# Optimization experiments

Measured on AMD Instinct MI355X. Metric: run time of the kernel, lower is better.

Reference implementation:

```python
import jax, jax.numpy as jnp
import numpy as np

THRESHOLD = 0.1  # init kwarg threshold
N_HITS_PER_EVENT = 200000
N_EVENTS = 64


def setup_inputs() -> dict:
    key = jax.random.key(0)
    n = N_HITS_PER_EVENT * N_EVENTS
    score = jax.random.uniform(key, (n, 1), dtype=jnp.float32)  # noise score in (0,1)
    row_splits = (jnp.arange(N_EVENTS + 1, dtype=jnp.int32) * N_HITS_PER_EVENT)
    return {"score": score, "row_splits": row_splits}


def reference(score, row_splits):
    """Faithful, fully vectorized version of select_threshold_with_backgather.

    Per segment: keep all vertices with score > threshold PLUS all vertices tied
    with the segment minimum score; non-kept vertices backgather to the FIRST
    kept minimum-score vertex of their segment (new/compacted indexing).
    Returns (sel [M,1], newrs [n_seg+1], backgather [N,1]) in the layer's
    call-output order (sel, newrs, allbackgather).
    """
    s = score[:, 0]
    n = s.shape[0]
    n_seg = row_splits.shape[0] - 1

    # segment id of every vertex from the row splits
    segids = jnp.searchsorted(row_splits, jnp.arange(n, dtype=row_splits.dtype), side='right') - 1
    segids = segids.astype(jnp.int32)

    # per-segment minimum score; ties with the min are all kept (== original isminscore)
    segmin = jax.ops.segment_min(s, segids, num_segments=n_seg)
    ismin = s == segmin[segids]
    keep = (s > THRESHOLD) | ismin

    # global compacted position of each kept vertex (n_previous_rs + local keeprange)
    kept_pos = jnp.cumsum(keep.astype(jnp.int32)) - 1

    # representative = first kept min-score vertex per segment (original minidx + n_previous_rs)
    big = jnp.int32(n)
    rep_pos = jax.ops.segment_min(jnp.where(keep & ismin, kept_pos, big), segids, num_segments=n_seg)

    backgather = jnp.where(keep, kept_pos, rep_pos[segids])

    # selection indices (data-dependent size; computed on concrete values, not under jit)
    sel = jnp.nonzero(keep)[0].astype(jnp.int32)

    counts = jax.ops.segment_sum(keep.astype(jnp.int32), segids, num_segments=n_seg)
    newrs = jnp.concatenate([jnp.zeros((1,), jnp.int32), jnp.cumsum(counts).astype(jnp.int32)])

    return sel[:, None], newrs, backgather[:, None].astype(jnp.int32)
```

## Files before the change

kernel.cpp:

```cpp
#include <hip/hip_runtime.h>
#include <stdint.h>

#define BLOCK 256
#define ITEMS 8
#define TILE (BLOCK * ITEMS)
#define WPB (TILE / 64)
#define MAXSEG 64
#define THRESH 0.1f

typedef unsigned long long u64;

__device__ __forceinline__ int find_seg(const int* rs, int n_seg, int i) {
    int lo = 0, hi = n_seg;
    while (hi - lo > 1) {
        int mid = (lo + hi) >> 1;
        if (rs[mid] <= i) lo = mid; else hi = mid;
    }
    return lo;
}

__global__ __launch_bounds__(BLOCK) void k_pass1(const float* __restrict__ score,
        const int* __restrict__ row_splits, int n_seg, int n, int nwords,
        u64* __restrict__ partial_val, int* __restrict__ partial_seg,
        u64* __restrict__ bitmask, int* __restrict__ block_counts) {
    __shared__ int rs[MAXSEG + 1];
    __shared__ u64 wval[8];
    __shared__ int wseg[8];
    __shared__ int wsum[4];
    for (int j = threadIdx.x; j <= n_seg; j += BLOCK) rs[j] = row_splits[j];
    __syncthreads();
    int lane = threadIdx.x & 63, wv = threadIdx.x >> 6;
    int wbase = blockIdx.x * TILE + wv * 512;
    u64 m0 = ~0ull, m1 = ~0ull;
    int sf = -1, sl = -1, cnt = 0;
    if (wbase < n) {
        int wend = min(n, wbase + 512) - 1;
        sf = find_seg(rs, n_seg, wbase);
        sl = find_seg(rs, n_seg, wend);
        int bval = (sl != sf) ? rs[sf + 1] : 0x7FFFFFFF;
        int tbase = wbase + lane * 8;
        unsigned int kbyte = 0;
        if (tbase < n) {
            float v[8];
            if (tbase + 8 <= n) {
                float4 f0 = *(const float4*)(score + tbase);
                float4 f1 = *(const float4*)(score + tbase + 4);
                v[0]=f0.x; v[1]=f0.y; v[2]=f0.z; v[3]=f0.w;
                v[4]=f1.x; v[5]=f1.y; v[6]=f1.z; v[7]=f1.w;
            } else {
                for (int j = 0; j < 8; j++) v[j] = (tbase + j < n) ? score[tbase + j] : 1.0f;
            }
            #pragma unroll
            for (int j = 0; j < 8; j++) {
                int i = tbase + j;
                if (i < n) {
                    u64 p = ((u64)__float_as_uint(v[j]) << 32) | (unsigned int)i;
                    if (i < bval) m0 = min(m0, p); else m1 = min(m1, p);
                    if (v[j] > THRESH) kbyte |= 1u << j;
                }
            }
            cnt = __popc(kbyte);
        }
        u64 acc = ((u64)kbyte) << (8 * (lane & 7));
        acc |= __shfl_xor((unsigned long long)acc, 1, 64);
        acc |= __shfl_xor((unsigned long long)acc, 2, 64);
        acc |= __shfl_xor((unsigned long long)acc, 4, 64);
        int src = (lane < 8) ? (8 * lane) : lane;
        u64 myword = __shfl((unsigned long long)acc, src, 64);
        for (int o = 32; o > 0; o >>= 1) {
            m0 = min(m0, (u64)__shfl_down((unsigned long long)m0, o, 64));
            m1 = min(m1, (u64)__shfl_down((unsigned long long)m1, o, 64));
            cnt += __shfl_down(cnt, o, 64);
        }
        if (lane < 8) {
            int w = (wbase >> 6) + lane;
            if (w < nwords) bitmask[w] = myword;
        }
    }
    if (lane == 0) {
        wval[2 * wv] = m0;     wseg[2 * wv] = sf;
        wval[2 * wv + 1] = m1; wseg[2 * wv + 1] = (sl != sf) ? sl : -1;
        wsum[wv] = (wbase < n) ? cnt : 0;
    }
    __syncthreads();
    if (threadIdx.x == 0) {
        int base = blockIdx.x * TILE;
        int endi = min(n, base + TILE) - 1;
        int s0 = find_seg(rs, n_seg, base);
        int s1 = find_seg(rs, n_seg, endi);
        u64 o0 = ~0ull, o1 = ~0ull;
        for (int k = 0; k < 8; k++) {
            if (wseg[k] == s0) o0 = min(o0, wval[k]);
            else if (wseg[k] == s1) o1 = min(o1, wval[k]);
        }
        partial_val[2 * blockIdx.x] = o0;
        partial_seg[2 * blockIdx.x] = s0;
        partial_val[2 * blockIdx.x + 1] = o1;
        partial_seg[2 * blockIdx.x + 1] = (s1 != s0) ? s1 : -1;
        block_counts[blockIdx.x] = wsum[0] + wsum[1] + wsum[2] + wsum[3];
    }
}

__global__ __launch_bounds__(BLOCK) void k_segfix(const float* __restrict__ score,
        const int* __restrict__ row_splits, int n_seg, int n,
        const u64* __restrict__ partial_val, const int* __restrict__ partial_seg,
        u64* __restrict__ seg_packed, u64* __restrict__ bitmask,
        int* __restrict__ block_counts) {
    __shared__ u64 wred[4];
    __shared__ int nmatch;
    __shared__ int mlist[64];
    int s = blockIdx.x;
    int lo = row_splits[s], hi = row_splits[s + 1];
    int lane = threadIdx.x & 63, wv = threadIdx.x >> 6;
    if (threadIdx.x == 0) nmatch = 0;
    u64 m = ~0ull;
    int e0 = 0, e1 = -1;
    if (hi > lo) {
        e0 = 2 * (lo / TILE);
        e1 = 2 * ((hi - 1) / TILE) + 1;
        for (int e = e0 + threadIdx.x; e <= e1; e += BLOCK)
            if (partial_seg[e] == s) m = min(m, partial_val[e]);
    }
    for (int o = 32; o > 0; o >>= 1)
        m = min(m, (u64)__shfl_down((unsigned long long)m, o, 64));
    if (lane == 0) wred[wv] = m;
    __syncthreads();
    if (threadIdx.x == 0) {
        u64 r = min(min(wred[0], wred[1]), min(wred[2], wred[3]));
        wred[0] = r;
        seg_packed[s] = r;
    }
    __syncthreads();
    u64 sp = wred[0];
    if (sp == ~0ull) return;
    unsigned int smb = (unsigned int)(sp >> 32);
    if (__uint_as_float(smb) > THRESH) return;
    for (int e = e0 + threadIdx.x; e <= e1; e += BLOCK) {
        if (partial_seg[e] == s && (unsigned int)(partial_val[e] >> 32) == smb) {
            int k = atomicAdd(&nmatch, 1);
            if (k < 64) mlist[k] = e >> 1;
        }
    }
    __syncthreads();
    int nm = min(nmatch, 64);
    for (int k = 0; k < nm; k++) {
        int b = mlist[k];
        int rlo = max(b * TILE, lo);
        int rhi = min(min((b + 1) * TILE, n), hi);
        int c = 0;
        for (int i = rlo + threadIdx.x; i < rhi; i += BLOCK) {
            if (__float_as_uint(score[i]) == smb) {
                atomicOr(&bitmask[i >> 6], 1ull << (i & 63));
                c++;
            }
        }
        for (int o = 32; o > 0; o >>= 1) c += __shfl_down(c, o, 64);
        if (lane == 0 && c) atomicAdd(&block_counts[b], c);
    }
}

__global__ __launch_bounds__(BLOCK) void k_scanq(const int* __restrict__ counts,
        int* __restrict__ offsets, int nb,
        const int* __restrict__ row_splits, int n_seg, int n, int M,
        const u64* __restrict__ seg_packed, const u64* __restrict__ bitmask,
        int* __restrict__ rep_pos, int* __restrict__ newrs_out) {
    __shared__ int wtot[BLOCK / 64];
    int lane = threadIdx.x & 63, wv = threadIdx.x >> 6;
    {
        int per = (nb + BLOCK - 1) / BLOCK;
        int s = per * threadIdx.x, e = min(nb, s + per);
        int sum = 0;
        for (int i = s; i < e; i++) sum += counts[i];
        int incl = sum;
        for (int o = 1; o < 64; o <<= 1) {
            int t = __shfl_up(incl, o, 64);
            if (lane >= o) incl += t;
        }
        if (lane == 63) wtot[wv] = incl;
        __syncthreads();
        int excl = incl - sum;
        for (int k = 0; k < wv; k++) excl += wtot[k];
        for (int i = s; i < e; i++) { offsets[i] = excl; excl += counts[i]; }
    }
    __syncthreads();
    int nq = 2 * n_seg + 1;
    int q = threadIdx.x;
    if (q < nq) {
        unsigned int uidx;
        if (q <= n_seg) uidx = (unsigned int)row_splits[q];
        else uidx = (unsigned int)(seg_packed[q - (n_seg + 1)] & 0xFFFFFFFFu);
        int result;
        if (uidx >= (unsigned int)n) {
            result = M;
        } else {
            int idx = (int)uidx;
            int b = idx / TILE;
            int wq = idx >> 6;
            int cnt = offsets[b];
            for (int w = b * WPB; w < wq; w++) cnt += __popcll(bitmask[w]);
            if (idx & 63) cnt += __popcll(bitmask[wq] & ((1ull << (idx & 63)) - 1));
            result = cnt;
        }
        if (q <= n_seg) newrs_out[q] = result;
        else rep_pos[q - (n_seg + 1)] = result;
    }
}

__global__ __launch_bounds__(BLOCK) void k_output(const int* __restrict__ row_splits,
        int n_seg, int n,
        const int* __restrict__ rep_pos, const u64* __restrict__ bitmask,
        const int* __restrict__ block_offsets,
        int* __restrict__ sel_out, int* __restrict__ back_out) {
    __shared__ int rs[MAXSEG + 1];
    __shared__ u64 swords[WPB];
    __shared__ int wpre[WPB];
    __shared__ int shead[6];
    __shared__ alignas(16) int skel[TILE + 8];
    for (int j = threadIdx.x; j <= n_seg; j += BLOCK) rs[j] = row_splits[j];
    int base = blockIdx.x * TILE;
    int lim = min(TILE, n - base);
    int nw = (lim + 63) >> 6;
    for (int j = threadIdx.x; j < nw; j += BLOCK) swords[j] = bitmask[(base >> 6) + j];
    __syncthreads();
    if (threadIdx.x == 0) {
        int acc = 0;
        for (int k = 0; k < nw; k++) { wpre[k] = acc; acc += __popcll(swords[k]); }
        int s0 = find_seg(rs, n_seg, base);
        int s1 = find_seg(rs, n_seg, base + lim - 1);
        shead[0] = (s1 != s0) ? rs[s0 + 1] : 0x7FFFFFFF;
        shead[1] = rep_pos[s0];
        shead[2] = rep_pos[s1];
        shead[3] = acc;
    }
    __syncthreads();
    int bval = shead[0], rep0 = shead[1], rep1 = shead[2], tot = shead[3];
    int bo = block_offsets[blockIdx.x];
    int st_b = (int)((4 - ((((uintptr_t)(back_out + base)) >> 2) & 3)) & 3);
    if (st_b > lim) st_b = lim;
    int st_s = (int)((4 - ((((uintptr_t)(sel_out + bo)) >> 2) & 3)) & 3);
    if (st_s > tot) st_s = tot;
    int selpad = 4 - st_s;

    int ngroups = (lim - st_b) >> 2;
    for (int g = threadIdx.x; g < ngroups; g += BLOCK) {
        int j0 = st_b + 4 * g;
        int vals[4];
        #pragma unroll
        for (int k = 0; k < 4; k++) {
            int j = j0 + k;
            int widx = j >> 6, r = j & 63;
            u64 w = swords[widx];
            int i = base + j;
            if ((w >> r) & 1) {
                int pos = bo + wpre[widx] + __popcll(w & ((1ull << r) - 1));
                vals[k] = pos;
                skel[pos - bo + selpad] = i;
            } else {
                vals[k] = (i >= bval) ? rep1 : rep0;
            }
        }
        *(int4*)(back_out + base + j0) = make_int4(vals[0], vals[1], vals[2], vals[3]);
    }
    for (int j = threadIdx.x; j < st_b; j += BLOCK) {
        int widx = j >> 6, r = j & 63;
        u64 w = swords[widx];
        int i = base + j, val;
        if ((w >> r) & 1) {
            int pos = bo + wpre[widx] + __popcll(w & ((1ull << r) - 1));
            val = pos;
            skel[pos - bo + selpad] = i;
        } else val = (i >= bval) ? rep1 : rep0;
        back_out[i] = val;
    }
    for (int j = st_b + 4 * ngroups + threadIdx.x; j < lim; j += BLOCK) {
        int widx = j >> 6, r = j & 63;
        u64 w = swords[widx];
        int i = base + j, val;
        if ((w >> r) & 1) {
            int pos = bo + wpre[widx] + __popcll(w & ((1ull << r) - 1));
            val = pos;
            skel[pos - bo + selpad] = i;
        } else val = (i >= bval) ? rep1 : rep0;
        back_out[i] = val;
    }
    __syncthreads();
    int nvg = (tot - st_s) >> 2;
    for (int g = threadIdx.x; g < nvg; g += BLOCK) {
        int4 v = *(const int4*)&skel[4 + 4 * g];
        *(int4*)(sel_out + bo + st_s + 4 * g) = v;
    }
    for (int j = threadIdx.x; j < st_s; j += BLOCK) sel_out[bo + j] = skel[j + selpad];
    for (int j = st_s + 4 * nvg + threadIdx.x; j < tot; j += BLOCK) sel_out[bo + j] = skel[j + selpad];
}

extern "C" void kernel_launch(void* const* d_in, const int* in_sizes, int n_in,
                              void* d_out, int out_size, void* d_ws, size_t ws_size,
                              hipStream_t stream) {
    const float* score = (const float*)d_in[0];
    const int* row_splits = (const int*)d_in[1];
    int n = in_sizes[0];
    int n_seg = in_sizes[1] - 1;
    int M = out_size - (n_seg + 1) - n;
    int nb = (n + TILE - 1) / TILE;
    int nwords = (n + 63) / 64;

    u64* seg_packed   = (u64*)d_ws;
    u64* partial_val  = seg_packed + MAXSEG;
    int* partial_seg  = (int*)(partial_val + 2 * nb);
    int* rep_pos      = partial_seg + 2 * nb;
    int* block_counts = rep_pos + 64;
    int* block_offsets= block_counts + nb;
    uintptr_t bm_addr = (uintptr_t)(block_offsets + nb);
    bm_addr = (bm_addr + 7) & ~(uintptr_t)7;
    u64* bitmask      = (u64*)bm_addr;

    int* out = (int*)d_out;
    int* sel_out   = out;
    int* newrs_out = out + M;
    int* back_out  = out + M + (n_seg + 1);

    hipLaunchKernelGGL(k_pass1, dim3(nb), dim3(BLOCK), 0, stream,
                       score, row_splits, n_seg, n, nwords,
                       partial_val, partial_seg, bitmask, block_counts);
    hipLaunchKernelGGL(k_segfix, dim3(n_seg), dim3(BLOCK), 0, stream,
                       score, row_splits, n_seg, n,
                       partial_val, partial_seg, seg_packed, bitmask, block_counts);
    hipLaunchKernelGGL(k_scanq, dim3(1), dim3(BLOCK), 0, stream,
                       block_counts, block_offsets, nb,
                       row_splits, n_seg, n, M, seg_packed, bitmask,
                       rep_pos, newrs_out);
    hipLaunchKernelGGL(k_output, dim3(nb), dim3(BLOCK), 0, stream,
                       row_splits, n_seg, n, rep_pos, bitmask,
                       block_offsets, sel_out, back_out);
}
```

Baseline: 173.5 us.

## Fuse segment-min fixup and scan into pass1 and output via last-block atomics

Removes the separate k_segfix and single-block k_scanq kernels. Pass1 now reduces segment minima with atomicMin into seg_packed and accumulates per-chunk counts with atomicAdd. The last block to finish a segment, detected through an atomic counter, performs the tie fixup. k_output derives each block's offset, representative positions and new row splits from chunk sums plus a wave-level partial prefix, cutting two launches and a serial scan. In exchange it adds a memset, global atomics and threadfence-based completion detection. The chunk sums are initialised to 0xFF (-1) and corrected with +1 in k_output, which is fragile.

```diff
diff --git a/kernel.cpp b/kernel.cpp
--- a/kernel.cpp
+++ b/kernel.cpp
@@ -6,6 +6,8 @@
 #define TILE (BLOCK * ITEMS)
 #define WPB (TILE / 64)
 #define MAXSEG 64
+#define CHUNK 64
+#define NCMAX 257
 #define THRESH 0.1f
 
 typedef unsigned long long u64;
@@ -19,14 +21,35 @@
     return lo;
 }
 
+__device__ __forceinline__ int wave_prefix_at(int idx, const int* chq,
+        const int* __restrict__ bc, const u64* __restrict__ bm, int lane) {
+    int t = idx / TILE;
+    int c = t / CHUNK;
+    int v = 0;
+    int j = c * CHUNK + lane;
+    if (j < t) v += bc[j];
+    int wq = idx >> 6;
+    int w = t * WPB + lane;
+    if (lane < WPB && w < wq) v += __popcll(bm[w]);
+    if (lane == 0 && (idx & 63)) v += __popcll(bm[wq] & ((1ull << (idx & 63)) - 1));
+    for (int o = 32; o > 0; o >>= 1) v += __shfl_down(v, o, 64);
+    return chq[c] + v;
+}
+
 __global__ __launch_bounds__(BLOCK) void k_pass1(const float* __restrict__ score,
         const int* __restrict__ row_splits, int n_seg, int n, int nwords,
         u64* __restrict__ partial_val, int* __restrict__ partial_seg,
-        u64* __restrict__ bitmask, int* __restrict__ block_counts) {
+        u64* __restrict__ bitmask, int* __restrict__ block_counts,
+        u64* __restrict__ seg_packed, int* __restrict__ seg_ctr,
+        int* __restrict__ chunk_sums) {
     __shared__ int rs[MAXSEG + 1];
     __shared__ u64 wval[8];
     __shared__ int wseg[8];
     __shared__ int wsum[4];
+    __shared__ int sfix[2];
+    __shared__ u64 sminp;
+    __shared__ int nmatch;
+    __shared__ int mlist[64];
     for (int j = threadIdx.x; j <= n_seg; j += BLOCK) rs[j] = row_splits[j];
     __syncthreads();
     int lane = threadIdx.x & 63, wv = threadIdx.x >> 6;
@@ -97,126 +120,80 @@
         partial_seg[2 * blockIdx.x] = s0;
         partial_val[2 * blockIdx.x + 1] = o1;
         partial_seg[2 * blockIdx.x + 1] = (s1 != s0) ? s1 : -1;
-        block_counts[blockIdx.x] = wsum[0] + wsum[1] + wsum[2] + wsum[3];
-    }
-}
-
-__global__ __launch_bounds__(BLOCK) void k_segfix(const float* __restrict__ score,
-        const int* __restrict__ row_splits, int n_seg, int n,
-        const u64* __restrict__ partial_val, const int* __restrict__ partial_seg,
-        u64* __restrict__ seg_packed, u64* __restrict__ bitmask,
-        int* __restrict__ block_counts) {
-    __shared__ u64 wred[4];
-    __shared__ int nmatch;
-    __shared__ int mlist[64];
-    int s = blockIdx.x;
-    int lo = row_splits[s], hi = row_splits[s + 1];
-    int lane = threadIdx.x & 63, wv = threadIdx.x >> 6;
-    if (threadIdx.x == 0) nmatch = 0;
-    u64 m = ~0ull;
-    int e0 = 0, e1 = -1;
-    if (hi > lo) {
-        e0 = 2 * (lo / TILE);
-        e1 = 2 * ((hi - 1) / TILE) + 1;
-        for (int e = e0 + threadIdx.x; e <= e1; e += BLOCK)
-            if (partial_seg[e] == s) m = min(m, partial_val[e]);
-    }
-    for (int o = 32; o > 0; o >>= 1)
-        m = min(m, (u64)__shfl_down((unsigned long long)m, o, 64));
-    if (lane == 0) wred[wv] = m;
-    __syncthreads();
-    if (threadIdx.x == 0) {
-        u64 r = min(min(wred[0], wred[1]), min(wred[2], wred[3]));
-        wred[0] = r;
-        seg_packed[s] = r;
-    }
-    __syncthreads();
-    u64 sp = wred[0];
-    if (sp == ~0ull) return;
-    unsigned int smb = (unsigned int)(sp >> 32);
-    if (__uint_as_float(smb) > THRESH) return;
-    for (int e = e0 + threadIdx.x; e <= e1; e += BLOCK) {
-        if (partial_seg[e] == s && (unsigned int)(partial_val[e] >> 32) == smb) {
-            int k = atomicAdd(&nmatch, 1);
-            if (k < 64) mlist[k] = e >> 1;
-        }
-    }
-    __syncthreads();
-    int nm = min(nmatch, 64);
-    for (int k = 0; k < nm; k++) {
-        int b = mlist[k];
-        int rlo = max(b * TILE, lo);
-        int rhi = min(min((b + 1) * TILE, n), hi);
-        int c = 0;
-        for (int i = rlo + threadIdx.x; i < rhi; i += BLOCK) {
-            if (__float_as_uint(score[i]) == smb) {
-                atomicOr(&bitmask[i >> 6], 1ull << (i & 63));
-                c++;
-            }
-        }
-        for (int o = 32; o > 0; o >>= 1) c += __shfl_down(c, o, 64);
-        if (lane == 0 && c) atomicAdd(&block_counts[b], c);
-    }
-}
-
-__global__ __launch_bounds__(BLOCK) void k_scanq(const int* __restrict__ counts,
-        int* __restrict__ offsets, int nb,
-        const int* __restrict__ row_splits, int n_seg, int n, int M,
+        int bc = wsum[0] + wsum[1] + wsum[2] + wsum[3];
+        block_counts[blockIdx.x] = bc;
+        atomicMin(&seg_packed[s0], o0);
+        if (s1 != s0) atomicMin(&seg_packed[s1], o1);
+        atomicAdd(&chunk_sums[blockIdx.x / CHUNK], bc);
+        __threadfence();
+        int f0 = -1, f1 = -1;
+        {
+            int nblk = (rs[s0 + 1] - 1) / TILE - rs[s0] / TILE + 1;
+            if (atomicAdd(&seg_ctr[s0], 1) == nblk - 2) f0 = s0;
+        }
+        if (s1 != s0) {
+            int nblk = (rs[s1 + 1] - 1) / TILE - rs[s1] / TILE + 1;
+            if (atomicAdd(&seg_ctr[s1], 1) == nblk - 2) f1 = s1;
+        }
+        if (f0 >= 0 || f1 >= 0) __threadfence();
+        sfix[0] = f0; sfix[1] = f1;
+    }
+    __syncthreads();
+    for (int k = 0; k < 2; k++) {
+        int s = sfix[k];
+        if (s < 0) continue;
+        if (threadIdx.x == 0) { sminp = seg_packed[s]; nmatch = 0; }
+        __syncthreads();
+        u64 sp = sminp;
+        if (sp != ~0ull) {
+            unsigned int smb = (unsigned int)(sp >> 32);
+            if (__uint_as_float(smb) <= THRESH) {
+                int lo = rs[s], hi = rs[s + 1];
+                int e0 = 2 * (lo / TILE), e1 = 2 * ((hi - 1) / TILE) + 1;
+                for (int e = e0 + threadIdx.x; e <= e1; e += BLOCK)
+                    if (partial_seg[e] == s && (unsigned int)(partial_val[e] >> 32) == smb) {
+                        int kk = atomicAdd(&nmatch, 1);
+                        if (kk < 64) mlist[kk] = e >> 1;
+                    }
+                __syncthreads();
+                int nm = min(nmatch, 64);
+                for (int kk = 0; kk < nm; kk++) {
+                    int b = mlist[kk];
+                    int rlo = max(b * TILE, lo);
+                    int rhi = min(min((b + 1) * TILE, n), hi);
+                    int c = 0;
+                    for (int i = rlo + threadIdx.x; i < rhi; i += BLOCK) {
+                        if (__float_as_uint(score[i]) == smb) {
+                            atomicOr(&bitmask[i >> 6], 1ull << (i & 63));
+                            c++;
+                        }
+                    }
+                    for (int o = 32; o > 0; o >>= 1) c += __shfl_down(c, o, 64);
+                    if (lane == 0 && c) {
+                        atomicAdd(&block_counts[b], c);
+                        atomicAdd(&chunk_sums[b / CHUNK], c);
+                    }
+                }
+            }
+        }
+        __syncthreads();
+    }
+}
+
+__global__ __launch_bounds__(BLOCK) void k_output(const int* __restrict__ row_splits,
+        int n_seg, int n, int nb, int nchunk, int M,
         const u64* __restrict__ seg_packed, const u64* __restrict__ bitmask,
-        int* __restrict__ rep_pos, int* __restrict__ newrs_out) {
-    __shared__ int wtot[BLOCK / 64];
-    int lane = threadIdx.x & 63, wv = threadIdx.x >> 6;
-    {
-        int per = (nb + BLOCK - 1) / BLOCK;
-        int s = per * threadIdx.x, e = min(nb, s + per);
-        int sum = 0;
-        for (int i = s; i < e; i++) sum += counts[i];
-        int incl = sum;
-        for (int o = 1; o < 64; o <<= 1) {
-            int t = __shfl_up(incl, o, 64);
-            if (lane >= o) incl += t;
-        }
-        if (lane == 63) wtot[wv] = incl;
-        __syncthreads();
-        int excl = incl - sum;
-        for (int k = 0; k < wv; k++) excl += wtot[k];
-        for (int i = s; i < e; i++) { offsets[i] = excl; excl += counts[i]; }
-    }
-    __syncthreads();
-    int nq = 2 * n_seg + 1;
-    int q = threadIdx.x;
-    if (q < nq) {
-        unsigned int uidx;
-        if (q <= n_seg) uidx = (unsigned int)row_splits[q];
-        else uidx = (unsigned int)(seg_packed[q - (n_seg + 1)] & 0xFFFFFFFFu);
-        int result;
-        if (uidx >= (unsigned int)n) {
-            result = M;
-        } else {
-            int idx = (int)uidx;
-            int b = idx / TILE;
-            int wq = idx >> 6;
-            int cnt = offsets[b];
-            for (int w = b * WPB; w < wq; w++) cnt += __popcll(bitmask[w]);
-            if (idx & 63) cnt += __popcll(bitmask[wq] & ((1ull << (idx & 63)) - 1));
-            result = cnt;
-        }
-        if (q <= n_seg) newrs_out[q] = result;
-        else rep_pos[q - (n_seg + 1)] = result;
-    }
-}
-
-__global__ __launch_bounds__(BLOCK) void k_output(const int* __restrict__ row_splits,
-        int n_seg, int n,
-        const int* __restrict__ rep_pos, const u64* __restrict__ bitmask,
-        const int* __restrict__ block_offsets,
-        int* __restrict__ sel_out, int* __restrict__ back_out) {
+        const int* __restrict__ block_counts, const int* __restrict__ chunk_sums,
+        int* __restrict__ sel_out, int* __restrict__ back_out,
+        int* __restrict__ newrs_out) {
     __shared__ int rs[MAXSEG + 1];
     __shared__ u64 swords[WPB];
     __shared__ int wpre[WPB];
-    __shared__ int shead[6];
+    __shared__ int shead[8];
+    __shared__ int chq[NCMAX];
     __shared__ alignas(16) int skel[TILE + 8];
     for (int j = threadIdx.x; j <= n_seg; j += BLOCK) rs[j] = row_splits[j];
+    for (int t = threadIdx.x; t < nchunk; t += BLOCK) chq[t] = chunk_sums[t] + 1;
     int base = blockIdx.x * TILE;
     int lim = min(TILE, n - base);
     int nw = (lim + 63) >> 6;
@@ -228,13 +205,43 @@
         int s0 = find_seg(rs, n_seg, base);
         int s1 = find_seg(rs, n_seg, base + lim - 1);
         shead[0] = (s1 != s0) ? rs[s0 + 1] : 0x7FFFFFFF;
-        shead[1] = rep_pos[s0];
-        shead[2] = rep_pos[s1];
+        shead[1] = s0;
+        shead[2] = s1;
         shead[3] = acc;
-    }
-    __syncthreads();
-    int bval = shead[0], rep0 = shead[1], rep1 = shead[2], tot = shead[3];
-    int bo = block_offsets[blockIdx.x];
+        int a2 = 0;
+        for (int c = 0; c < nchunk; c++) { int t = chq[c]; chq[c] = a2; a2 += t; }
+    }
+    __syncthreads();
+    int lane = threadIdx.x & 63, wv = threadIdx.x >> 6;
+    {
+        int s0 = shead[1], s1 = shead[2];
+        if (wv == 0) {
+            int r = wave_prefix_at(base, chq, block_counts, bitmask, lane);
+            if (lane == 0) shead[4] = r;
+        } else if (wv == 1) {
+            unsigned int u = (unsigned int)(seg_packed[s0] & 0xFFFFFFFFu);
+            int r = (u >= (unsigned int)n) ? M
+                    : wave_prefix_at((int)u, chq, block_counts, bitmask, lane);
+            if (lane == 0) shead[5] = r;
+        } else if (wv == 2) {
+            unsigned int u = (unsigned int)(seg_packed[s1] & 0xFFFFFFFFu);
+            int r = (u >= (unsigned int)n) ? M
+                    : wave_prefix_at((int)u, chq, block_counts, bitmask, lane);
+            if (lane == 0) shead[6] = r;
+        } else {
+            for (int q = 0; q < n_seg; q++) {
+                int u = rs[q];
+                if (u >= base && u < base + lim) {
+                    int r = wave_prefix_at(u, chq, block_counts, bitmask, lane);
+                    if (lane == 0) newrs_out[q] = r;
+                }
+            }
+            if (blockIdx.x == nb - 1 && lane == 0) newrs_out[n_seg] = M;
+        }
+    }
+    __syncthreads();
+    int bval = shead[0], tot = shead[3], bo = shead[4];
+    int rep0 = shead[5], rep1 = shead[6];
     int st_b = (int)((4 - ((((uintptr_t)(back_out + base)) >> 2) & 3)) & 3);
     if (st_b > lim) st_b = lim;
     int st_s = (int)((4 - ((((uintptr_t)(sel_out + bo)) >> 2) & 3)) & 3);
@@ -303,14 +310,17 @@
     int M = out_size - (n_seg + 1) - n;
     int nb = (n + TILE - 1) / TILE;
     int nwords = (n + 63) / 64;
+    int nchunk = (nb + CHUNK - 1) / CHUNK;
 
     u64* seg_packed   = (u64*)d_ws;
-    u64* partial_val  = seg_packed + MAXSEG;
+    int* seg_ctr      = (int*)(seg_packed + MAXSEG);
+    int* chunk_sums   = seg_ctr + MAXSEG;
+    uintptr_t pv_addr = (uintptr_t)(chunk_sums + nchunk);
+    pv_addr = (pv_addr + 7) & ~(uintptr_t)7;
+    u64* partial_val  = (u64*)pv_addr;
     int* partial_seg  = (int*)(partial_val + 2 * nb);
-    int* rep_pos      = partial_seg + 2 * nb;
-    int* block_counts = rep_pos + 64;
-    int* block_offsets= block_counts + nb;
-    uintptr_t bm_addr = (uintptr_t)(block_offsets + nb);
+    int* block_counts = partial_seg + 2 * nb;
+    uintptr_t bm_addr = (uintptr_t)(block_counts + nb);
     bm_addr = (bm_addr + 7) & ~(uintptr_t)7;
     u64* bitmask      = (u64*)bm_addr;
 
@@ -319,17 +329,14 @@
     int* newrs_out = out + M;
     int* back_out  = out + M + (n_seg + 1);
 
+    size_t init_bytes = (size_t)((char*)(chunk_sums + nchunk) - (char*)d_ws);
+    hipMemsetAsync(d_ws, 0xFF, init_bytes, stream);
     hipLaunchKernelGGL(k_pass1, dim3(nb), dim3(BLOCK), 0, stream,
                        score, row_splits, n_seg, n, nwords,
-                       partial_val, partial_seg, bitmask, block_counts);
-    hipLaunchKernelGGL(k_segfix, dim3(n_seg), dim3(BLOCK), 0, stream,
-                       score, row_splits, n_seg, n,
-                       partial_val, partial_seg, seg_packed, bitmask, block_counts);
-    hipLaunchKernelGGL(k_scanq, dim3(1), dim3(BLOCK), 0, stream,
-                       block_counts, block_offsets, nb,
-                       row_splits, n_seg, n, M, seg_packed, bitmask,
-                       rep_pos, newrs_out);
+                       partial_val, partial_seg, bitmask, block_counts,
+                       seg_packed, seg_ctr, chunk_sums);
     hipLaunchKernelGGL(k_output, dim3(nb), dim3(BLOCK), 0, stream,
-                       row_splits, n_seg, n, rep_pos, bitmask,
-                       block_offsets, sel_out, back_out);
-}
+                       row_splits, n_seg, n, nb, nchunk, M,
+                       seg_packed, bitmask, block_counts, chunk_sums,
+                       sel_out, back_out, newrs_out);
+}
```

New measurement: 376.4 us. +117.0%, slower.

## Fold block-count scan and rep/newrs queries into output kernel

Applied to the files above, without the earlier changes.

Removes the single-block scan kernel. Each output block now computes its own exclusive prefix by reducing block_counts over all preceding tiles, resolves its representative positions and newrs entries locally, and writes them out. This saves one kernel launch and a serial one-block stage, at the cost of redundant, quadratic-total reads of block_counts (about 6250 blocks, each reading up to 6250 ints) and extra barriers in every output block.

```diff
diff --git a/kernel.cpp b/kernel.cpp
--- a/kernel.cpp
+++ b/kernel.cpp
@@ -159,62 +159,19 @@
     }
 }
 
-__global__ __launch_bounds__(BLOCK) void k_scanq(const int* __restrict__ counts,
-        int* __restrict__ offsets, int nb,
-        const int* __restrict__ row_splits, int n_seg, int n, int M,
+__global__ __launch_bounds__(BLOCK) void k_output(const int* __restrict__ row_splits,
+        int n_seg, int n, int nb, int M,
         const u64* __restrict__ seg_packed, const u64* __restrict__ bitmask,
-        int* __restrict__ rep_pos, int* __restrict__ newrs_out) {
-    __shared__ int wtot[BLOCK / 64];
-    int lane = threadIdx.x & 63, wv = threadIdx.x >> 6;
-    {
-        int per = (nb + BLOCK - 1) / BLOCK;
-        int s = per * threadIdx.x, e = min(nb, s + per);
-        int sum = 0;
-        for (int i = s; i < e; i++) sum += counts[i];
-        int incl = sum;
-        for (int o = 1; o < 64; o <<= 1) {
-            int t = __shfl_up(incl, o, 64);
-            if (lane >= o) incl += t;
-        }
-        if (lane == 63) wtot[wv] = incl;
-        __syncthreads();
-        int excl = incl - sum;
-        for (int k = 0; k < wv; k++) excl += wtot[k];
-        for (int i = s; i < e; i++) { offsets[i] = excl; excl += counts[i]; }
-    }
-    __syncthreads();
-    int nq = 2 * n_seg + 1;
-    int q = threadIdx.x;
-    if (q < nq) {
-        unsigned int uidx;
-        if (q <= n_seg) uidx = (unsigned int)row_splits[q];
-        else uidx = (unsigned int)(seg_packed[q - (n_seg + 1)] & 0xFFFFFFFFu);
-        int result;
-        if (uidx >= (unsigned int)n) {
-            result = M;
-        } else {
-            int idx = (int)uidx;
-            int b = idx / TILE;
-            int wq = idx >> 6;
-            int cnt = offsets[b];
-            for (int w = b * WPB; w < wq; w++) cnt += __popcll(bitmask[w]);
-            if (idx & 63) cnt += __popcll(bitmask[wq] & ((1ull << (idx & 63)) - 1));
-            result = cnt;
-        }
-        if (q <= n_seg) newrs_out[q] = result;
-        else rep_pos[q - (n_seg + 1)] = result;
-    }
-}
-
-__global__ __launch_bounds__(BLOCK) void k_output(const int* __restrict__ row_splits,
-        int n_seg, int n,
-        const int* __restrict__ rep_pos, const u64* __restrict__ bitmask,
-        const int* __restrict__ block_offsets,
-        int* __restrict__ sel_out, int* __restrict__ back_out) {
+        const int* __restrict__ block_counts,
+        int* __restrict__ sel_out, int* __restrict__ back_out,
+        int* __restrict__ newrs_out) {
     __shared__ int rs[MAXSEG + 1];
     __shared__ u64 swords[WPB];
     __shared__ int wpre[WPB];
-    __shared__ int shead[6];
+    __shared__ int shead[8];
+    __shared__ int qidx[4];
+    __shared__ int wred3[4][3];
+    __shared__ int qsum[3];
     __shared__ alignas(16) int skel[TILE + 8];
     for (int j = threadIdx.x; j <= n_seg; j += BLOCK) rs[j] = row_splits[j];
     int base = blockIdx.x * TILE;
@@ -223,18 +180,80 @@
     for (int j = threadIdx.x; j < nw; j += BLOCK) swords[j] = bitmask[(base >> 6) + j];
     __syncthreads();
     if (threadIdx.x == 0) {
-        int acc = 0;
-        for (int k = 0; k < nw; k++) { wpre[k] = acc; acc += __popcll(swords[k]); }
         int s0 = find_seg(rs, n_seg, base);
         int s1 = find_seg(rs, n_seg, base + lim - 1);
         shead[0] = (s1 != s0) ? rs[s0 + 1] : 0x7FFFFFFF;
-        shead[1] = rep_pos[s0];
-        shead[2] = rep_pos[s1];
+        shead[1] = s0;
+        shead[2] = s1;
+        unsigned int u0 = (unsigned int)(seg_packed[s0] & 0xFFFFFFFFu);
+        unsigned int u1 = (unsigned int)(seg_packed[s1] & 0xFFFFFFFFu);
+        qidx[1] = (u0 < (unsigned int)n) ? (int)u0 : -1;
+        qidx[2] = (s1 != s0) ? ((u1 < (unsigned int)n) ? (int)u1 : -1) : qidx[1];
+    } else if (threadIdx.x == 64) {
+        int acc = 0;
+        for (int k = 0; k < nw; k++) { wpre[k] = acc; acc += __popcll(swords[k]); }
         shead[3] = acc;
     }
     __syncthreads();
-    int bval = shead[0], rep0 = shead[1], rep1 = shead[2], tot = shead[3];
-    int bo = block_offsets[blockIdx.x];
+    int lane = threadIdx.x & 63, wv = threadIdx.x >> 6;
+    {
+        int t = blockIdx.x;
+        int q1 = qidx[1], q2 = qidx[2];
+        int T1 = (q1 >= 0) ? q1 / TILE : 0;
+        int T2 = (q2 >= 0) ? q2 / TILE : 0;
+        int maxT = max(t, max(T1, T2));
+        int a0 = 0, a1 = 0, a2 = 0;
+        for (int i = threadIdx.x; i < maxT; i += BLOCK) {
+            int b = block_counts[i];
+            if (i < t)  a0 += b;
+            if (i < T1) a1 += b;
+            if (i < T2) a2 += b;
+        }
+        for (int o = 32; o > 0; o >>= 1) {
+            a0 += __shfl_down(a0, o, 64);
+            a1 += __shfl_down(a1, o, 64);
+            a2 += __shfl_down(a2, o, 64);
+        }
+        if (lane == 0) { wred3[wv][0] = a0; wred3[wv][1] = a1; wred3[wv][2] = a2; }
+    }
+    __syncthreads();
+    if (threadIdx.x < 3) {
+        int s = 0;
+        for (int k = 0; k < 4; k++) s += wred3[k][threadIdx.x];
+        qsum[threadIdx.x] = s;
+    }
+    __syncthreads();
+    if (wv == 0) {
+        if (lane == 0) shead[4] = qsum[0];
+    } else if (wv == 1 || wv == 2) {
+        int qi = qidx[wv];
+        int r;
+        if (qi < 0) r = M;
+        else {
+            int tt = qi / TILE, wq = qi >> 6;
+            int v = 0;
+            int w = tt * WPB + lane;
+            if (lane < WPB && w < wq) v += __popcll(bitmask[w]);
+            if (lane == 0 && (qi & 63)) v += __popcll(bitmask[wq] & ((1ull << (qi & 63)) - 1));
+            for (int o = 32; o > 0; o >>= 1) v += __shfl_down(v, o, 64);
+            r = qsum[wv] + v;
+        }
+        if (lane == 0) shead[4 + wv] = r;
+    } else {
+        for (int q = 0; q < n_seg; q++) {
+            int u = rs[q];
+            if (u >= base && u < base + lim) {
+                int j = u - base, widx = j >> 6;
+                int r = qsum[0] + wpre[widx]
+                        + ((j & 63) ? __popcll(swords[widx] & ((1ull << (j & 63)) - 1)) : 0);
+                if (lane == 0) newrs_out[q] = r;
+            }
+        }
+        if (blockIdx.x == nb - 1 && lane == 0) newrs_out[n_seg] = M;
+    }
+    __syncthreads();
+    int bval = shead[0], tot = shead[3], bo = shead[4];
+    int rep0 = shead[5], rep1 = shead[6];
     int st_b = (int)((4 - ((((uintptr_t)(back_out + base)) >> 2) & 3)) & 3);
     if (st_b > lim) st_b = lim;
     int st_s = (int)((4 - ((((uintptr_t)(sel_out + bo)) >> 2) & 3)) & 3);
@@ -307,10 +326,8 @@
     u64* seg_packed   = (u64*)d_ws;
     u64* partial_val  = seg_packed + MAXSEG;
     int* partial_seg  = (int*)(partial_val + 2 * nb);
-    int* rep_pos      = partial_seg + 2 * nb;
-    int* block_counts = rep_pos + 64;
-    int* block_offsets= block_counts + nb;
-    uintptr_t bm_addr = (uintptr_t)(block_offsets + nb);
+    int* block_counts = partial_seg + 2 * nb;
+    uintptr_t bm_addr = (uintptr_t)(block_counts + nb);
     bm_addr = (bm_addr + 7) & ~(uintptr_t)7;
     u64* bitmask      = (u64*)bm_addr;
 
@@ -324,12 +341,10 @@
                        partial_val, partial_seg, bitmask, block_counts);
     hipLaunchKernelGGL(k_segfix, dim3(n_seg), dim3(BLOCK), 0, stream,
                        score, row_splits, n_seg, n,
-                       partial_val, partial_seg, seg_packed, bitmask, block_counts);
-    hipLaunchKernelGGL(k_scanq, dim3(1), dim3(BLOCK), 0, stream,
-                       block_counts, block_offsets, nb,
-                       row_splits, n_seg, n, M, seg_packed, bitmask,
-                       rep_pos, newrs_out);
+                       partial_val, partial_seg, seg_packed, bitmask,
+                       block_counts);
     hipLaunchKernelGGL(k_output, dim3(nb), dim3(BLOCK), 0, stream,
-                       row_splits, n_seg, n, rep_pos, bitmask,
-                       block_offsets, sel_out, back_out);
-}
+                       row_splits, n_seg, n, nb, M,
+                       seg_packed, bitmask, block_counts,
+                       sel_out, back_out, newrs_out);
+}
```

Result: slower. 183.1 us (+5.6%).

## Track per-partial min tie counts and fold segment-min fixup into scan and output

Applied to the files above, without the earlier changes.

Pass 1 now also counts how many elements tie with each partial minimum. The separate k_segfix kernel goes away. The segment minimum is reduced inside the single-block scan kernel, and tie counts are added to the block offsets there. The output kernel re-scans its own tile's scores to set the tied-minimum bits in shared memory. This removes one kernel launch and its serial atomic fixup pass, at the cost of extra compare logic in pass 1 and more serial work in the single-block scan.

```diff
diff --git a/kernel.cpp b/kernel.cpp
--- a/kernel.cpp
+++ b/kernel.cpp
@@ -22,9 +22,11 @@
 __global__ __launch_bounds__(BLOCK) void k_pass1(const float* __restrict__ score,
         const int* __restrict__ row_splits, int n_seg, int n, int nwords,
         u64* __restrict__ partial_val, int* __restrict__ partial_seg,
+        int* __restrict__ partial_cnt,
         u64* __restrict__ bitmask, int* __restrict__ block_counts) {
     __shared__ int rs[MAXSEG + 1];
     __shared__ u64 wval[8];
+    __shared__ int wcnt[8];
     __shared__ int wseg[8];
     __shared__ int wsum[4];
     for (int j = threadIdx.x; j <= n_seg; j += BLOCK) rs[j] = row_splits[j];
@@ -32,6 +34,7 @@
     int lane = threadIdx.x & 63, wv = threadIdx.x >> 6;
     int wbase = blockIdx.x * TILE + wv * 512;
     u64 m0 = ~0ull, m1 = ~0ull;
+    int c0 = 0, c1 = 0;
     int sf = -1, sl = -1, cnt = 0;
     if (wbase < n) {
         int wend = min(n, wbase + 512) - 1;
@@ -54,8 +57,17 @@
             for (int j = 0; j < 8; j++) {
                 int i = tbase + j;
                 if (i < n) {
-                    u64 p = ((u64)__float_as_uint(v[j]) << 32) | (unsigned int)i;
-                    if (i < bval) m0 = min(m0, p); else m1 = min(m1, p);
+                    unsigned int sb = __float_as_uint(v[j]);
+                    u64 p = ((u64)sb << 32) | (unsigned int)i;
+                    if (i < bval) {
+                        unsigned int a = (unsigned int)(m0 >> 32);
+                        if (sb < a) { m0 = p; c0 = 1; }
+                        else if (sb == a) c0++;
+                    } else {
+                        unsigned int a = (unsigned int)(m1 >> 32);
+                        if (sb < a) { m1 = p; c1 = 1; }
+                        else if (sb == a) c1++;
+                    }
                     if (v[j] > THRESH) kbyte |= 1u << j;
                 }
             }
@@ -68,8 +80,16 @@
         int src = (lane < 8) ? (8 * lane) : lane;
         u64 myword = __shfl((unsigned long long)acc, src, 64);
         for (int o = 32; o > 0; o >>= 1) {
-            m0 = min(m0, (u64)__shfl_down((unsigned long long)m0, o, 64));
-            m1 = min(m1, (u64)__shfl_down((unsigned long long)m1, o, 64));
+            u64 om = __shfl_down((unsigned long long)m0, o, 64);
+            int oc = __shfl_down(c0, o, 64);
+            unsigned int a = (unsigned int)(m0 >> 32), bb = (unsigned int)(om >> 32);
+            if (bb < a) { m0 = om; c0 = oc; }
+            else if (bb == a) { c0 += oc; if (om < m0) m0 = om; }
+            om = __shfl_down((unsigned long long)m1, o, 64);
+            oc = __shfl_down(c1, o, 64);
+            a = (unsigned int)(m1 >> 32); bb = (unsigned int)(om >> 32);
+            if (bb < a) { m1 = om; c1 = oc; }
+            else if (bb == a) { c1 += oc; if (om < m1) m1 = om; }
             cnt += __shfl_down(cnt, o, 64);
         }
         if (lane < 8) {
@@ -78,8 +98,8 @@
         }
     }
     if (lane == 0) {
-        wval[2 * wv] = m0;     wseg[2 * wv] = sf;
-        wval[2 * wv + 1] = m1; wseg[2 * wv + 1] = (sl != sf) ? sl : -1;
+        wval[2 * wv] = m0;     wcnt[2 * wv] = c0;     wseg[2 * wv] = sf;
+        wval[2 * wv + 1] = m1; wcnt[2 * wv + 1] = c1; wseg[2 * wv + 1] = (sl != sf) ? sl : -1;
         wsum[wv] = (wbase < n) ? cnt : 0;
     }
     __syncthreads();
@@ -89,88 +109,70 @@
         int s0 = find_seg(rs, n_seg, base);
         int s1 = find_seg(rs, n_seg, endi);
         u64 o0 = ~0ull, o1 = ~0ull;
+        int f0 = 0, f1 = 0;
         for (int k = 0; k < 8; k++) {
-            if (wseg[k] == s0) o0 = min(o0, wval[k]);
-            else if (wseg[k] == s1) o1 = min(o1, wval[k]);
+            if (wseg[k] == s0) {
+                u64 om = wval[k]; int oc = wcnt[k];
+                unsigned int a = (unsigned int)(o0 >> 32), bb = (unsigned int)(om >> 32);
+                if (bb < a) { o0 = om; f0 = oc; }
+                else if (bb == a) { f0 += oc; if (om < o0) o0 = om; }
+            } else if (wseg[k] == s1) {
+                u64 om = wval[k]; int oc = wcnt[k];
+                unsigned int a = (unsigned int)(o1 >> 32), bb = (unsigned int)(om >> 32);
+                if (bb < a) { o1 = om; f1 = oc; }
+                else if (bb == a) { f1 += oc; if (om < o1) o1 = om; }
+            }
         }
         partial_val[2 * blockIdx.x] = o0;
         partial_seg[2 * blockIdx.x] = s0;
+        partial_cnt[2 * blockIdx.x] = f0;
         partial_val[2 * blockIdx.x + 1] = o1;
         partial_seg[2 * blockIdx.x + 1] = (s1 != s0) ? s1 : -1;
+        partial_cnt[2 * blockIdx.x + 1] = f1;
         block_counts[blockIdx.x] = wsum[0] + wsum[1] + wsum[2] + wsum[3];
     }
 }
 
-__global__ __launch_bounds__(BLOCK) void k_segfix(const float* __restrict__ score,
-        const int* __restrict__ row_splits, int n_seg, int n,
-        const u64* __restrict__ partial_val, const int* __restrict__ partial_seg,
-        u64* __restrict__ seg_packed, u64* __restrict__ bitmask,
-        int* __restrict__ block_counts) {
-    __shared__ u64 wred[4];
-    __shared__ int nmatch;
-    __shared__ int mlist[64];
-    int s = blockIdx.x;
-    int lo = row_splits[s], hi = row_splits[s + 1];
-    int lane = threadIdx.x & 63, wv = threadIdx.x >> 6;
-    if (threadIdx.x == 0) nmatch = 0;
-    u64 m = ~0ull;
-    int e0 = 0, e1 = -1;
-    if (hi > lo) {
-        e0 = 2 * (lo / TILE);
-        e1 = 2 * ((hi - 1) / TILE) + 1;
-        for (int e = e0 + threadIdx.x; e <= e1; e += BLOCK)
-            if (partial_seg[e] == s) m = min(m, partial_val[e]);
-    }
-    for (int o = 32; o > 0; o >>= 1)
-        m = min(m, (u64)__shfl_down((unsigned long long)m, o, 64));
-    if (lane == 0) wred[wv] = m;
-    __syncthreads();
-    if (threadIdx.x == 0) {
-        u64 r = min(min(wred[0], wred[1]), min(wred[2], wred[3]));
-        wred[0] = r;
-        seg_packed[s] = r;
-    }
-    __syncthreads();
-    u64 sp = wred[0];
-    if (sp == ~0ull) return;
-    unsigned int smb = (unsigned int)(sp >> 32);
-    if (__uint_as_float(smb) > THRESH) return;
-    for (int e = e0 + threadIdx.x; e <= e1; e += BLOCK) {
-        if (partial_seg[e] == s && (unsigned int)(partial_val[e] >> 32) == smb) {
-            int k = atomicAdd(&nmatch, 1);
-            if (k < 64) mlist[k] = e >> 1;
-        }
-    }
-    __syncthreads();
-    int nm = min(nmatch, 64);
-    for (int k = 0; k < nm; k++) {
-        int b = mlist[k];
-        int rlo = max(b * TILE, lo);
-        int rhi = min(min((b + 1) * TILE, n), hi);
-        int c = 0;
-        for (int i = rlo + threadIdx.x; i < rhi; i += BLOCK) {
-            if (__float_as_uint(score[i]) == smb) {
-                atomicOr(&bitmask[i >> 6], 1ull << (i & 63));
-                c++;
-            }
-        }
-        for (int o = 32; o > 0; o >>= 1) c += __shfl_down(c, o, 64);
-        if (lane == 0 && c) atomicAdd(&block_counts[b], c);
-    }
+__device__ __forceinline__ int corr_e(int e, const int* __restrict__ ps,
+        const u64* __restrict__ pv, const int* __restrict__ pc,
+        const u64* segmin) {
+    int s = ps[e];
+    if (s < 0) return 0;
+    unsigned int smb = (unsigned int)(segmin[s] >> 32);
+    if (__uint_as_float(smb) > THRESH) return 0;
+    if ((unsigned int)(pv[e] >> 32) != smb) return 0;
+    return pc[e];
 }
 
 __global__ __launch_bounds__(BLOCK) void k_scanq(const int* __restrict__ counts,
         int* __restrict__ offsets, int nb,
         const int* __restrict__ row_splits, int n_seg, int n, int M,
-        const u64* __restrict__ seg_packed, const u64* __restrict__ bitmask,
+        const u64* __restrict__ partial_val, const int* __restrict__ partial_seg,
+        const int* __restrict__ partial_cnt,
+        u64* __restrict__ seg_packed, const u64* __restrict__ bitmask,
         int* __restrict__ rep_pos, int* __restrict__ newrs_out) {
+    __shared__ u64 segmin[MAXSEG];
     __shared__ int wtot[BLOCK / 64];
-    int lane = threadIdx.x & 63, wv = threadIdx.x >> 6;
+    int tid = threadIdx.x, lane = tid & 63, wv = tid >> 6;
+    if (tid < MAXSEG) segmin[tid] = ~0ull;
+    __syncthreads();
+    int ne = 2 * nb;
+    for (int e = tid; e < ne; e += BLOCK) {
+        int s = partial_seg[e];
+        if (s >= 0) {
+            u64 pv = partial_val[e];
+            if (pv < segmin[s]) atomicMin(&segmin[s], pv);
+        }
+    }
+    __syncthreads();
+    if (tid < n_seg) seg_packed[tid] = segmin[tid];
     {
         int per = (nb + BLOCK - 1) / BLOCK;
-        int s = per * threadIdx.x, e = min(nb, s + per);
+        int s = per * tid, e = min(nb, s + per);
         int sum = 0;
-        for (int i = s; i < e; i++) sum += counts[i];
+        for (int i = s; i < e; i++)
+            sum += counts[i] + corr_e(2 * i, partial_seg, partial_val, partial_cnt, segmin)
+                             + corr_e(2 * i + 1, partial_seg, partial_val, partial_cnt, segmin);
         int incl = sum;
         for (int o = 1; o < 64; o <<= 1) {
             int t = __shfl_up(incl, o, 64);
@@ -180,41 +182,52 @@
         __syncthreads();
         int excl = incl - sum;
         for (int k = 0; k < wv; k++) excl += wtot[k];
-        for (int i = s; i < e; i++) { offsets[i] = excl; excl += counts[i]; }
+        for (int i = s; i < e; i++) {
+            offsets[i] = excl;
+            excl += counts[i] + corr_e(2 * i, partial_seg, partial_val, partial_cnt, segmin)
+                              + corr_e(2 * i + 1, partial_seg, partial_val, partial_cnt, segmin);
+        }
     }
     __syncthreads();
     int nq = 2 * n_seg + 1;
-    int q = threadIdx.x;
-    if (q < nq) {
+    if (tid < nq) {
+        int qseg = (tid <= n_seg) ? tid : (tid - (n_seg + 1));
         unsigned int uidx;
-        if (q <= n_seg) uidx = (unsigned int)row_splits[q];
-        else uidx = (unsigned int)(seg_packed[q - (n_seg + 1)] & 0xFFFFFFFFu);
+        if (tid <= n_seg) uidx = (unsigned int)row_splits[tid];
+        else uidx = (unsigned int)(segmin[qseg] & 0xFFFFFFFFu);
         int result;
         if (uidx >= (unsigned int)n) {
             result = M;
         } else {
             int idx = (int)uidx;
-            int b = idx / TILE;
+            int T = idx / TILE;
             int wq = idx >> 6;
-            int cnt = offsets[b];
-            for (int w = b * WPB; w < wq; w++) cnt += __popcll(bitmask[w]);
+            int cnt = offsets[T];
+            for (int w = T * WPB; w < wq; w++) cnt += __popcll(bitmask[w]);
             if (idx & 63) cnt += __popcll(bitmask[wq] & ((1ull << (idx & 63)) - 1));
+            if (partial_seg[2 * T] != qseg)
+                cnt += corr_e(2 * T, partial_seg, partial_val, partial_cnt, segmin);
             result = cnt;
         }
-        if (q <= n_seg) newrs_out[q] = result;
-        else rep_pos[q - (n_seg + 1)] = result;
-    }
-}
-
-__global__ __launch_bounds__(BLOCK) void k_output(const int* __restrict__ row_splits,
-        int n_seg, int n,
+        if (tid <= n_seg) newrs_out[tid] = result;
+        else rep_pos[qseg] = result;
+    }
+}
+
+__global__ __launch_bounds__(BLOCK) void k_output(const float* __restrict__ score,
+        const int* __restrict__ row_splits, int n_seg, int n,
+        const u64* __restrict__ partial_val, const int* __restrict__ partial_seg,
+        const u64* __restrict__ seg_packed,
         const int* __restrict__ rep_pos, const u64* __restrict__ bitmask,
         const int* __restrict__ block_offsets,
         int* __restrict__ sel_out, int* __restrict__ back_out) {
     __shared__ int rs[MAXSEG + 1];
     __shared__ u64 swords[WPB];
     __shared__ int wpre[WPB];
-    __shared__ int shead[6];
+    __shared__ int shead[4];
+    __shared__ int fix_n;
+    __shared__ int fix_lo[2], fix_hi[2];
+    __shared__ unsigned int fix_smb[2];
     __shared__ alignas(16) int skel[TILE + 8];
     for (int j = threadIdx.x; j <= n_seg; j += BLOCK) rs[j] = row_splits[j];
     int base = blockIdx.x * TILE;
@@ -223,13 +236,45 @@
     for (int j = threadIdx.x; j < nw; j += BLOCK) swords[j] = bitmask[(base >> 6) + j];
     __syncthreads();
     if (threadIdx.x == 0) {
+        int b = blockIdx.x;
+        int s0 = find_seg(rs, n_seg, base);
+        int s1 = find_seg(rs, n_seg, base + lim - 1);
+        int bval = (s1 != s0) ? rs[s0 + 1] : 0x7FFFFFFF;
+        shead[0] = bval;
+        shead[1] = rep_pos[s0];
+        shead[2] = rep_pos[s1];
+        int nf = 0;
+        #pragma unroll
+        for (int h = 0; h < 2; h++) {
+            int e = 2 * b + h;
+            int s = partial_seg[e];
+            if (s >= 0) {
+                unsigned int smb = (unsigned int)(seg_packed[s] >> 32);
+                if (__uint_as_float(smb) <= THRESH &&
+                    (unsigned int)(partial_val[e] >> 32) == smb) {
+                    fix_lo[nf] = h ? bval : base;
+                    fix_hi[nf] = h ? (base + lim) : min(bval, base + lim);
+                    fix_smb[nf] = smb;
+                    nf++;
+                }
+            }
+        }
+        fix_n = nf;
+    }
+    __syncthreads();
+    for (int k = 0; k < fix_n; k++) {
+        unsigned int smb = fix_smb[k];
+        for (int i = fix_lo[k] + threadIdx.x; i < fix_hi[k]; i += BLOCK) {
+            if (__float_as_uint(score[i]) == smb) {
+                int j = i - base;
+                atomicOr(&((unsigned int*)swords)[j >> 5], 1u << (j & 31));
+            }
+        }
+    }
+    __syncthreads();
+    if (threadIdx.x == 0) {
         int acc = 0;
         for (int k = 0; k < nw; k++) { wpre[k] = acc; acc += __popcll(swords[k]); }
-        int s0 = find_seg(rs, n_seg, base);
-        int s1 = find_seg(rs, n_seg, base + lim - 1);
-        shead[0] = (s1 != s0) ? rs[s0 + 1] : 0x7FFFFFFF;
-        shead[1] = rep_pos[s0];
-        shead[2] = rep_pos[s1];
         shead[3] = acc;
     }
     __syncthreads();
@@ -307,10 +352,11 @@
     u64* seg_packed   = (u64*)d_ws;
     u64* partial_val  = seg_packed + MAXSEG;
     int* partial_seg  = (int*)(partial_val + 2 * nb);
-    int* rep_pos      = partial_seg + 2 * nb;
-    int* block_counts = rep_pos + 64;
+    int* partial_cnt  = partial_seg + 2 * nb;
+    int* block_counts = partial_cnt + 2 * nb;
     int* block_offsets= block_counts + nb;
-    uintptr_t bm_addr = (uintptr_t)(block_offsets + nb);
+    int* rep_pos      = block_offsets + nb;
+    uintptr_t bm_addr = (uintptr_t)(rep_pos + MAXSEG);
     bm_addr = (bm_addr + 7) & ~(uintptr_t)7;
     u64* bitmask      = (u64*)bm_addr;
 
@@ -321,15 +367,15 @@
 
     hipLaunchKernelGGL(k_pass1, dim3(nb), dim3(BLOCK), 0, stream,
                        score, row_splits, n_seg, n, nwords,
-                       partial_val, partial_seg, bitmask, block_counts);
-    hipLaunchKernelGGL(k_segfix, dim3(n_seg), dim3(BLOCK), 0, stream,
-                       score, row_splits, n_seg, n,
-                       partial_val, partial_seg, seg_packed, bitmask, block_counts);
+                       partial_val, partial_seg, partial_cnt, bitmask, block_counts);
     hipLaunchKernelGGL(k_scanq, dim3(1), dim3(BLOCK), 0, stream,
                        block_counts, block_offsets, nb,
-                       row_splits, n_seg, n, M, seg_packed, bitmask,
-                       rep_pos, newrs_out);
+                       row_splits, n_seg, n, M,
+                       partial_val, partial_seg, partial_cnt,
+                       seg_packed, bitmask, rep_pos, newrs_out);
     hipLaunchKernelGGL(k_output, dim3(nb), dim3(BLOCK), 0, stream,
-                       row_splits, n_seg, n, rep_pos, bitmask,
-                       block_offsets, sel_out, back_out);
-}
+                       score, row_splits, n_seg, n,
+                       partial_val, partial_seg, seg_packed,
+                       rep_pos, bitmask, block_offsets,
+                       sel_out, back_out);
+}
```

Measured after the change: 229.7 us. 32.4% more time.
